# Performance work log

Hardware: AMD Instinct MI355X
Metric: run time of the kernel (lower is better)

The kernel has to match this reference:

```python
import jax, jax.numpy as jnp
import numpy as np

N = 1 << 20   # number of values to quantize
K = 256       # codebook size (8-bit)


def setup_inputs() -> dict:
    key = jax.random.key(0)
    kx, kc = jax.random.split(key)
    x = jax.random.normal(kx, (N,), dtype=jnp.float32)
    centers = jax.random.normal(kc, (K,), dtype=jnp.float32)
    return {"x": x, "centers": centers}


def reference(x, centers):
    # (x[:, None] - centers[None, :]).abs().argmin(dim=1)
    # -> index of nearest scalar codebook entry per element, shape (N,)
    diff = jnp.abs(x[:, None] - centers[None, :])  # (N, K)
    return jnp.argmin(diff, axis=1)
```

## Files before the change

kernel.cpp:

```cpp
#include <hip/hip_runtime.h>

#define N_ELEM (1 << 20)
#define K 256
#define BLOCK 256
#define EPT 4
#define GRID (N_ELEM / (BLOCK * EPT))



__global__ __launch_bounds__(K) void sort_centers_kernel(
    const float* __restrict__ centers,
    float* __restrict__ ws_val,
    int*   __restrict__ ws_idx)
{
    __shared__ float sc[K];
    const int t = threadIdx.x;
    const float c = centers[t];
    sc[t] = c;
    __syncthreads();

    int rank = 0;
#pragma unroll 8
    for (int j = 0; j < K; ++j) {
        float cj = sc[j];
        rank += (cj < c) || (cj == c && j < t);
    }
    ws_val[rank] = c;
    ws_idx[rank] = t;
}

__global__ __launch_bounds__(BLOCK) void argmin_bsearch_kernel(
    const float* __restrict__ x,
    const float* __restrict__ ws_val,
    const int*   __restrict__ ws_idx,
    int*         __restrict__ out)
{
    __shared__ float s_val[K];
    __shared__ int   s_idx[K];
    const int t = threadIdx.x;
    s_val[t] = ws_val[t];
    s_idx[t] = ws_idx[t];
    __syncthreads();

    const int base = (blockIdx.x * BLOCK + t) * EPT;
    float4 v = *reinterpret_cast<const float4*>(x + base);
    float xs[EPT] = {v.x, v.y, v.z, v.w};
    int res[EPT];

#pragma unroll
    for (int e = 0; e < EPT; ++e) {
        const float xv = xs[e];
        int pos = 0;
#pragma unroll
        for (int s = 128; s > 0; s >>= 1)
            pos += (s_val[pos + s - 1] < xv) ? s : 0;
        pos += (s_val[pos] < xv) ? 1 : 0;

        const int il = (pos > 0)  ? pos - 1 : 0;
        const int ir = (pos < K)  ? pos     : K - 1;
        const float dl = fabsf(xv - s_val[il]);
        const float dr = fabsf(xv - s_val[ir]);
        const int ol = s_idx[il], orr = s_idx[ir];
        res[e] = (dl < dr) ? ol : ((dr < dl) ? orr : min(ol, orr));
    }

    *reinterpret_cast<int4*>(out + base) = make_int4(res[0], res[1], res[2], res[3]);
}

extern "C" void kernel_launch(void* const* d_in, const int* in_sizes, int n_in,
                              void* d_out, int out_size, void* d_ws, size_t ws_size,
                              hipStream_t stream)
{
    const float* x       = (const float*)d_in[0];
    const float* centers = (const float*)d_in[1];
    int*         out     = (int*)d_out;

    float* ws_val = (float*)d_ws;
    int*   ws_idx = (int*)(ws_val + K);

    sort_centers_kernel<<<1, K, 0, stream>>>(centers, ws_val, ws_idx);
    argmin_bsearch_kernel<<<GRID, BLOCK, 0, stream>>>(x, ws_val, ws_idx, out);
}
```

Measured before the change: 67.40 us.

## Resolve top search levels in registers and swizzle shared-memory sorted centers

The sort kernel now also writes every 16th sorted center into a small top-level table. The search kernel loads those 16 values into registers and resolves the first four binary-search levels with register selects, leaving only five shared-memory probes per element instead of nine. Shared indices are XOR-swizzled to spread bank conflicts from divergent probe addresses, and the rank loop reads centers as float4. The select trees add ALU work and registers, and the search runs on a workload that already looks memory-bound.

New measurement: 67.65 us. About the same (+0.4%).

```diff
diff --git a/kernel.cpp b/kernel.cpp
--- a/kernel.cpp
+++ b/kernel.cpp
@@ -11,55 +11,86 @@
 __global__ __launch_bounds__(K) void sort_centers_kernel(
     const float* __restrict__ centers,
     float* __restrict__ ws_val,
-    int*   __restrict__ ws_idx)
+    int*   __restrict__ ws_idx,
+    float* __restrict__ ws_top)
 {
-    __shared__ float sc[K];
+    __shared__ __align__(16) float sc[K];
     const int t = threadIdx.x;
     const float c = centers[t];
     sc[t] = c;
     __syncthreads();
 
     int rank = 0;
+    const float4* sc4 = reinterpret_cast<const float4*>(sc);
 #pragma unroll 8
-    for (int j = 0; j < K; ++j) {
-        float cj = sc[j];
-        rank += (cj < c) || (cj == c && j < t);
+    for (int q = 0; q < K / 4; ++q) {
+        const float4 v = sc4[q];
+        const int j = q * 4;
+        rank += (v.x < c) || (v.x == c && (j + 0) < t);
+        rank += (v.y < c) || (v.y == c && (j + 1) < t);
+        rank += (v.z < c) || (v.z == c && (j + 2) < t);
+        rank += (v.w < c) || (v.w == c && (j + 3) < t);
     }
     ws_val[rank] = c;
     ws_idx[rank] = t;
+    if ((rank & 15) == 15) ws_top[rank >> 4] = c;
 }
 
 __global__ __launch_bounds__(BLOCK) void argmin_bsearch_kernel(
     const float* __restrict__ x,
     const float* __restrict__ ws_val,
     const int*   __restrict__ ws_idx,
+    const float* __restrict__ ws_top,
     int*         __restrict__ out)
 {
     __shared__ float s_val[K];
     __shared__ int   s_idx[K];
     const int t = threadIdx.x;
-    s_val[t] = ws_val[t];
+    s_val[t ^ (t >> 5)] = ws_val[t];
     s_idx[t] = ws_idx[t];
+
+    const float4 tA = *reinterpret_cast<const float4*>(ws_top + 0);
+    const float4 tB = *reinterpret_cast<const float4*>(ws_top + 4);
+    const float4 tC = *reinterpret_cast<const float4*>(ws_top + 8);
+    const float4 tD = *reinterpret_cast<const float4*>(ws_top + 12);
     __syncthreads();
 
     const int base = (blockIdx.x * BLOCK + t) * EPT;
-    float4 v = *reinterpret_cast<const float4*>(x + base);
+    const float4 v = *reinterpret_cast<const float4*>(x + base);
     float xs[EPT] = {v.x, v.y, v.z, v.w};
     int res[EPT];
 
 #pragma unroll
     for (int e = 0; e < EPT; ++e) {
         const float xv = xs[e];
-        int pos = 0;
+
+        const bool c1 = tB.w < xv;
+        const float v2 = c1 ? tC.w : tA.w;
+        const bool c2 = v2 < xv;
+        const float v3 = c1 ? (c2 ? tD.y : tC.y)
+                            : (c2 ? tB.y : tA.y);
+        const bool c3 = v3 < xv;
+        const float v4 = c1 ? (c2 ? (c3 ? tD.z : tD.x)
+                                  : (c3 ? tC.z : tC.x))
+                            : (c2 ? (c3 ? tB.z : tB.x)
+                                  : (c3 ? tA.z : tA.x));
+        const bool c4 = v4 < xv;
+        int pos = ((((((int)c1 << 1) | (int)c2) << 1 | (int)c3) << 1) | (int)c4) << 4;
+
 #pragma unroll
-        for (int s = 128; s > 0; s >>= 1)
-            pos += (s_val[pos + s - 1] < xv) ? s : 0;
-        pos += (s_val[pos] < xv) ? 1 : 0;
+        for (int s = 8; s > 0; s >>= 1) {
+            const int p = pos + s - 1;
+            pos += (s_val[p ^ (p >> 5)] < xv) ? s : 0;
+        }
+        {
+            const int p = pos;
+            pos += (s_val[p ^ (p >> 5)] < xv) ? 1 : 0;
+        }
 
-        const int il = (pos > 0)  ? pos - 1 : 0;
-        const int ir = (pos < K)  ? pos     : K - 1;
-        const float dl = fabsf(xv - s_val[il]);
-        const float dr = fabsf(xv - s_val[ir]);
+        const int il = (pos > 0) ? pos - 1 : 0;
+        const int ir = (pos < K) ? pos : K - 1;
+        const float dl = fabsf(xv - s_val[il ^ (il >> 5)]);
+        const float dr = fabsf(xv - s_val[ir ^ (ir >> 5)]);
         const int ol = s_idx[il], orr = s_idx[ir];
         res[e] = (dl < dr) ? ol : ((dr < dl) ? orr : min(ol, orr));
     }
@@ -77,7 +108,8 @@
 
     float* ws_val = (float*)d_ws;
     int*   ws_idx = (int*)(ws_val + K);
+    float* ws_top = (float*)(ws_idx + K);
 
-    sort_centers_kernel<<<1, K, 0, stream>>>(centers, ws_val, ws_idx);
-    argmin_bsearch_kernel<<<GRID, BLOCK, 0, stream>>>(x, ws_val, ws_idx, out);
+    sort_centers_kernel<<<1, K, 0, stream>>>(centers, ws_val, ws_idx, ws_top);
+    argmin_bsearch_kernel<<<GRID, BLOCK, 0, stream>>>(x, ws_val, ws_idx, ws_top, out);
 }
```
